# Performance work log

Measured on AMD Instinct MI355X. Metric: run time of the kernel, lower is better.

Reference implementation:

```python
import jax, jax.numpy as jnp
import numpy as np
import math

RCR = 5.2
RCA = 3.5
NUM_SPECIES = 4


def _triu_index(num_species):
    s1, s2 = np.triu_indices(num_species)
    ret = np.zeros((num_species, num_species), dtype=np.int32)
    ret[s1, s2] = np.arange(len(s1))
    ret[s2, s1] = np.arange(len(s1))
    return ret


def _cutoff_cosine(d, rc):
    return 0.5 * jnp.cos(d * (math.pi / rc)) + 0.5


def setup_inputs():
    key = jax.random.key(0)
    k1, k2 = jax.random.split(key)
    M, A = 32, 48
    BOX = 8.0  # ~0.43 atoms/A^3, realistic organic density
    coordinates = jax.random.uniform(k1, (M, A, 3), dtype=jnp.float32) * BOX
    species = jax.random.randint(k2, (M, A), 0, NUM_SPECIES)
    EtaR = jnp.array([16.0], dtype=jnp.float32)
    ShfR = jnp.asarray(0.9 + (RCR - 0.9) / 16.0 * np.arange(16), dtype=jnp.float32)
    EtaA = jnp.array([8.0], dtype=jnp.float32)
    Zeta = jnp.array([32.0], dtype=jnp.float32)
    ShfA = jnp.asarray(0.9 + (RCA - 0.9) / 4.0 * np.arange(4), dtype=jnp.float32)
    ShfZ = jnp.asarray((np.arange(8) + 0.5) * np.pi / 8.0, dtype=jnp.float32)
    return {"coordinates": coordinates, "EtaR": EtaR, "ShfR": ShfR,
            "EtaA": EtaA, "Zeta": Zeta, "ShfA": ShfA, "ShfZ": ShfZ,
            "species": species}


def _compute_aev(coordinates, EtaR, ShfR, EtaA, Zeta, ShfA, ShfZ, species):
    M, A, _ = coordinates.shape
    S = NUM_SPECIES
    npairs_sp = S * (S + 1) // 2  # 10 unordered species pairs
    rad_sub = EtaR.shape[0] * ShfR.shape[0]   # 16
    ang_sub = EtaA.shape[0] * Zeta.shape[0] * ShfA.shape[0] * ShfZ.shape[0]  # 32

    diff = coordinates[:, :, None, :] - coordinates[:, None, :, :]  # (M,A,A,3)
    D = jnp.linalg.norm(diff, axis=-1)                              # (M,A,A)
    mrow = jnp.arange(M)[:, None]

    # ---------- radial AEV (eq. 3) ----------
    p1, p2 = np.triu_indices(A, 1)                                  # static (P,)
    d = D[:, p1, p2]                                                # (M,P)
    mask_r = (d <= RCR).astype(d.dtype)
    du = d[:, :, None, None]                                        # (M,P,1,1)
    fc = _cutoff_cosine(du, RCR)
    rt = 0.25 * jnp.exp(-EtaR[:, None] * (du - ShfR[None, :]) ** 2) * fc
    rt = (rt * mask_r[:, :, None, None]).reshape(M, len(p1), rad_sub)
    sp = species
    idx1 = p1[None, :] * S + sp[:, p2]                              # (M,P)
    idx2 = p2[None, :] * S + sp[:, p1]
    radial = jnp.zeros((M, A * S, rad_sub), dtype=rt.dtype)
    radial = radial.at[mrow, idx1].add(rt).at[mrow, idx2].add(rt)
    radial = radial.reshape(M, A, S * rad_sub)

    # ---------- angular AEV (eq. 4) ----------
    # static triple list: central atom i with unordered neighbor pair (j,k), j,k != i
    jj, kk = np.triu_indices(A - 1, 1)
    tri = []
    for i in range(A):
        others = np.concatenate([np.arange(i), np.arange(i + 1, A)])
        tri.append(np.stack([np.full(jj.shape, i), others[jj], others[kk]], 1))
    tri = np.concatenate(tri)                                       # (T,3)
    ci, n1, n2 = tri[:, 0], tri[:, 1], tri[:, 2]

    v1 = coordinates[:, n1] - coordinates[:, ci]                    # (M,T,3)
    v2 = coordinates[:, n2] - coordinates[:, ci]
    d1 = D[:, ci, n1]
    d2 = D[:, ci, n2]
    mask_a = ((d1 <= RCA) & (d2 <= RCA)).astype(d1.dtype)           # (M,T)
    eps = 1e-8  # torch cosine_similarity eps
    cos = 0.95 * jnp.sum(v1 * v2, -1) / (jnp.maximum(d1, eps) * jnp.maximum(d2, eps))
    ang = jnp.arccos(cos)                                           # (M,T)

    # broadcast axes: (M, T, EtaA, Zeta, ShfA, ShfZ) as in torchani constants
    EtaA_b = EtaA.reshape(1, 1, -1, 1, 1, 1)
    Zeta_b = Zeta.reshape(1, 1, 1, -1, 1, 1)
    ShfA_b = ShfA.reshape(1, 1, 1, 1, -1, 1)
    ShfZ_b = ShfZ.reshape(1, 1, 1, 1, 1, -1)
    a6 = ang[:, :, None, None, None, None]
    dm = ((d1 + d2) / 2)[:, :, None, None, None, None]
    fcj = (_cutoff_cosine(d1, RCA) * _cutoff_cosine(d2, RCA))[:, :, None, None, None, None]
    f1 = ((1 + jnp.cos(a6 - ShfZ_b)) / 2) ** Zeta_b
    f2 = jnp.exp(-EtaA_b * (dm - ShfA_b) ** 2)
    at = (2 * f1 * f2 * fcj).reshape(M, tri.shape[0], ang_sub)
    at = at * mask_a[:, :, None]

    triu = jnp.asarray(_triu_index(S))
    pidx = triu[sp[:, n1], sp[:, n2]]                               # (M,T)
    flat = ci[None, :] * npairs_sp + pidx
    angular = jnp.zeros((M, A * npairs_sp, ang_sub), dtype=at.dtype)
    angular = angular.at[mrow, flat].add(at).reshape(M, A, npairs_sp * ang_sub)

    return jnp.concatenate([radial, angular], axis=-1)              # (M,A,384)


def reference(coordinates, EtaR, ShfR, EtaA, Zeta, ShfA, ShfZ, species):
    return _compute_aev(coordinates, EtaR, ShfR, EtaA, Zeta, ShfA, ShfZ, species)
```

## Files before the change

kernel.cpp:

```cpp
#include <hip/hip_runtime.h>
#include <hip/hip_bf16.h>


#define NA 48
#define RCR_F 5.2f
#define RCA_F 3.5f
#define PI_F 3.14159265358979f
#define LOG2E_F 1.44269504088896f
#define RADLEN 64
#define AEVLEN 384

#define WAVE_SYNC() do { asm volatile("s_waitcnt lgkmcnt(0)" ::: "memory"); \
                         __builtin_amdgcn_sched_barrier(0); } while (0)

struct Smem {
    float sx[NA], sy[NA], sz[NA];
    int   ssp[NA];
    float ra[NA]; unsigned rbu[NA];
    float ad[NA], avx[NA], avy[NA], avz[NA], afc[NA]; int asp[NA];
    float4 pstage[4][64];
    int    sortidx[4][64];
    float rpart[4][64];
    float apart[4][320];
};

template <typename T> __device__ __forceinline__ float toF(const T* p, int i);
template <> __device__ __forceinline__ float toF<float>(const float* p, int i) { return p[i]; }
template <> __device__ __forceinline__ float toF<__hip_bfloat16>(const __hip_bfloat16* p, int i) { return __bfloat162float(p[i]); }

template <typename T> __device__ __forceinline__ void stF(T* p, size_t i, float v);
template <> __device__ __forceinline__ void stF<float>(float* p, size_t i, float v) { p[i] = v; }
template <> __device__ __forceinline__ void stF<__hip_bfloat16>(__hip_bfloat16* p, size_t i, float v) { p[i] = __float2bfloat16(v); }

__device__ __forceinline__ int triu_idx(int a, int b) {
    int lo = a < b ? a : b;
    int hi = a < b ? b : a;
    return lo * 4 - (lo * (lo - 1)) / 2 + (hi - lo);
}

template <typename T>
__device__ void aev_body(Smem& sm,
    const T* __restrict__ coords, const T* __restrict__ etaR_p,
    const T* __restrict__ shfR_p, const T* __restrict__ etaA_p,
    const T* __restrict__ zeta_p, const T* __restrict__ shfA_p,
    const T* __restrict__ shfZ_p, const int* __restrict__ species,
    T* __restrict__ out)
{
    const int tid  = threadIdx.x;
    const int lane = tid & 63;
    const int w    = tid >> 6;
    const int bid  = blockIdx.x;
    const int m  = bid / NA;
    const int ci = bid % NA;

    const float etaR = toF(etaR_p, 0);
    const float etaA = toF(etaA_p, 0);
    const float zeta = toF(zeta_p, 0);
    const float kR   = etaR * LOG2E_F;
    const float k2   = etaA * LOG2E_F;

    if (tid < NA) {
        int g = m * NA + tid;
        sm.sx[tid]  = toF(coords, 3 * g + 0);
        sm.sy[tid]  = toF(coords, 3 * g + 1);
        sm.sz[tid]  = toF(coords, 3 * g + 2);
        sm.ssp[tid] = species[g];
    }
    __syncthreads();

    const float cx = sm.sx[ci], cy = sm.sy[ci], cz = sm.sz[ci];
    float dx = 0.f, dy = 0.f, dz = 0.f, d = 1e30f;
    if (lane < NA && lane != ci) {
        dx = sm.sx[lane] - cx; dy = sm.sy[lane] - cy; dz = sm.sz[lane] - cz;
        d = sqrtf(dx * dx + dy * dy + dz * dz);
    }
    const unsigned long long mRm = __ballot(d <= RCR_F);
    const unsigned long long mAm = __ballot(d <= RCA_F);
    const unsigned long long lanebit = 1ull << lane;
    const unsigned long long below = lanebit - 1ull;
    if (w == 0 && (mRm & lanebit)) {
        int s = __popcll(mRm & below);
        float fcR = 0.5f * __cosf(d * (PI_F / RCR_F)) + 0.5f;
        float rb = fmaxf(__log2f(0.25f * fcR) - kR * d * d, -8.0e4f);
        sm.ra[s]  = 2.f * kR * d;
        sm.rbu[s] = (__float_as_uint(rb) & ~3u) | (unsigned)sm.ssp[lane];
    }
    if (w == 1 && (mAm & lanebit)) {
        int s = __popcll(mAm & below);
        sm.ad[s]  = d;
        sm.avx[s] = dx; sm.avy[s] = dy; sm.avz[s] = dz;
        sm.afc[s] = 0.5f * __cosf(d * (PI_F / RCA_F)) + 0.5f;
        sm.asp[s] = sm.ssp[lane];
    }
    const int nR  = (int)__popcll(mRm);
    const int nAn = (int)__popcll(mAm);
    __syncthreads();

    const float myShfR = toF(shfR_p, lane & 15);
    const int   mySp   = lane >> 4;
    const float myRc   = kR * myShfR * myShfR;
    float racc = 0.f;
    for (int i = w; i < nR; i += 4) {
        unsigned ru = sm.rbu[i];
        float arg = __builtin_fmaf(sm.ra[i], myShfR, __uint_as_float(ru)) - myRc;
        float t = __builtin_amdgcn_exp2f(arg);
        racc += ((int)(ru & 3u) == mySp) ? t : 0.f;
    }
    sm.rpart[w][lane] = racc;

    const int myA = (lane >> 3) & 3;
    const int myZ = lane & 7;
    const int p0  = lane >> 5;
    const float myShfA = toF(shfA_p, myA);
    const float myShfZ = toF(shfZ_p, myZ);
    const float myCz = __cosf(myShfZ);
    const float mySz = __sinf(myShfZ);
    const float myLc = k2 * myShfA * myShfA;
    const bool  z32  = (zeta == 32.f);

    float accs[5] = {0.f, 0.f, 0.f, 0.f, 0.f};
    const int np = nAn * (nAn - 1) / 2;

    for (int base = 64 * w; base < np; base += 256) {
        const int nc = (np - base < 64) ? (np - base) : 64;
        const bool active = lane < nc;
        int myrow = -1;
        if (active) {
            int p = base + lane;
            const int b = 2 * nAn - 1;
            float sq = sqrtf((float)(b * b - 8 * p));
            int j = (int)(((float)b - sq) * 0.5f);
            if ((j + 1) * (b - 1 - j) <= 2 * p) j++;
            if (j * (b - j) > 2 * p) j--;
            int k = p - ((j * (b - j)) >> 1) + j + 1;

            float d1 = sm.ad[j], d2 = sm.ad[k];
            float dot = sm.avx[j] * sm.avx[k] + sm.avy[j] * sm.avy[k] + sm.avz[j] * sm.avz[k];
            float cv = 0.95f * dot / (fmaxf(d1, 1e-8f) * fmaxf(d2, 1e-8f));
            float sv = sqrtf(fmaxf(1.f - cv * cv, 0.f));
            float dm = 0.5f * (d1 + d2);
            float fc2 = 2.f * sm.afc[j] * sm.afc[k];
            float pe = fmaxf(-k2 * dm * dm + __log2f(fc2), -8.0e4f);
            float pd = 2.f * k2 * dm;
            sm.pstage[w][lane] = make_float4(cv, sv, pd, pe);
            myrow = triu_idx(sm.asp[j], sm.asp[k]);
        }

        int cnt[10], st[10];
        {
            int run = 0, rank = 0, stmy = 0;
            #pragma unroll
            for (int r = 0; r < 10; ++r) {
                unsigned long long bm = __ballot(myrow == r);
                bool mine = (myrow == r);
                rank = mine ? (int)__popcll(bm & below) : rank;
                stmy = mine ? run : stmy;
                st[r]  = run;
                cnt[r] = (int)__popcll(bm);
                run += cnt[r];
            }
            if (active) sm.sortidx[w][stmy + rank] = lane;
        }
        WAVE_SYNC();

        #pragma unroll
        for (int u = 0; u < 5; ++u) {
            const int cnE = cnt[2 * u], cnO = cnt[2 * u + 1];
            const int stE = st[2 * u],  stO = st[2 * u + 1];
            const int cnMy = p0 ? cnO : cnE;
            const int stMy = p0 ? stO : stE;
            const int trips = cnE > cnO ? cnE : cnO;
            for (int o = 0; o < trips; ++o) {
                bool valid = o < cnMy;
                int idx = valid ? (stMy + o) : 0;
                int q = sm.sortidx[w][idx];
                float4 P = sm.pstage[w][q];
                float cd = __builtin_fmaf(P.x, myCz, P.y * mySz);
                float x = __builtin_fmaf(0.5f, cd, 0.5f);
                float f1;
                if (z32) { float x2 = x*x, x4 = x2*x2, x8 = x4*x4, x16 = x8*x8; f1 = x16*x16; }
                else     { f1 = __powf(x, zeta); }
                float term = f1 * __builtin_amdgcn_exp2f(
                                 __builtin_fmaf(P.z, myShfA, P.w - myLc));
                accs[u] += valid ? term : 0.f;
            }
        }
        WAVE_SYNC();
    }

    sm.apart[w][lane + 0]   = accs[0];
    sm.apart[w][lane + 64]  = accs[1];
    sm.apart[w][lane + 128] = accs[2];
    sm.apart[w][lane + 192] = accs[3];
    sm.apart[w][lane + 256] = accs[4];
    __syncthreads();

    const size_t ob = (size_t)bid * AEVLEN;
    if (tid < 64) {
        float r = sm.rpart[0][tid] + sm.rpart[1][tid] + sm.rpart[2][tid] + sm.rpart[3][tid];
        stF(out, ob + tid, r);
    }
    {
        float v = sm.apart[0][tid] + sm.apart[1][tid] + sm.apart[2][tid] + sm.apart[3][tid];
        stF(out, ob + RADLEN + tid, v);
    }
    if (tid < 64) {
        int s = 256 + tid;
        float v = sm.apart[0][s] + sm.apart[1][s] + sm.apart[2][s] + sm.apart[3][s];
        stF(out, ob + RADLEN + s, v);
    }
}

__global__ __launch_bounds__(256) void aev_kernel(
    const void* coords, const void* etaR, const void* shfR, const void* etaA,
    const void* zeta, const void* shfA, const void* shfZ,
    const int* __restrict__ species, void* out)
{
    __shared__ Smem sm;
    const float probe = __uint_as_float(((const unsigned int*)shfR)[0]);
    if (probe > 0.85f && probe < 0.95f) {
        aev_body<float>(sm, (const float*)coords, (const float*)etaR,
                        (const float*)shfR, (const float*)etaA, (const float*)zeta,
                        (const float*)shfA, (const float*)shfZ, species, (float*)out);
    } else {
        aev_body<__hip_bfloat16>(sm, (const __hip_bfloat16*)coords,
                        (const __hip_bfloat16*)etaR, (const __hip_bfloat16*)shfR,
                        (const __hip_bfloat16*)etaA, (const __hip_bfloat16*)zeta,
                        (const __hip_bfloat16*)shfA, (const __hip_bfloat16*)shfZ,
                        species, (__hip_bfloat16*)out);
    }
}

extern "C" void kernel_launch(void* const* d_in, const int* in_sizes, int n_in,
                              void* d_out, int out_size, void* d_ws, size_t ws_size,
                              hipStream_t stream) {
    aev_kernel<<<dim3(32 * NA), dim3(256), 0, stream>>>(
        d_in[0], d_in[1], d_in[2], d_in[3], d_in[4], d_in[5], d_in[6],
        (const int*)d_in[7], d_out);
}
```

Measured before the change: 79.79 us.

## Pack LDS neighbor data into vector structs and write sorted pair params directly

Replaces the separate per-field LDS arrays with packed float2/float4 records, and takes the center-atom coordinates by wave shuffle from registers instead of staging through LDS, which removes one block barrier. Pair parameters are now written straight into their species-sorted slot, dropping the sortidx indirection and one dependent LDS read per inner iteration. Pairs are also interleaved across waves (p = base + 4*lane + w) to balance the tail. This cuts LDS traffic and latency in the angular loop, at the cost of wider LDS accesses and a changed order of the pair work.

```diff
diff --git a/kernel.cpp b/kernel.cpp
--- a/kernel.cpp
+++ b/kernel.cpp
@@ -14,14 +14,12 @@
                          __builtin_amdgcn_sched_barrier(0); } while (0)
 
 struct Smem {
-    float sx[NA], sy[NA], sz[NA];
-    int   ssp[NA];
-    float ra[NA]; unsigned rbu[NA];
-    float ad[NA], avx[NA], avy[NA], avz[NA], afc[NA]; int asp[NA];
+    float2 rr[NA];
+    float4 aj[NA];
+    float2 af[NA];
     float4 pstage[4][64];
-    int    sortidx[4][64];
-    float rpart[4][64];
-    float apart[4][320];
+    float  rpart[4][64];
+    float  apart[4][320];
 };
 
 template <typename T> __device__ __forceinline__ float toF(const T* p, int i);
@@ -59,19 +57,21 @@
     const float kR   = etaR * LOG2E_F;
     const float k2   = etaA * LOG2E_F;
 
-    if (tid < NA) {
-        int g = m * NA + tid;
-        sm.sx[tid]  = toF(coords, 3 * g + 0);
-        sm.sy[tid]  = toF(coords, 3 * g + 1);
-        sm.sz[tid]  = toF(coords, 3 * g + 2);
-        sm.ssp[tid] = species[g];
-    }
-    __syncthreads();
-
-    const float cx = sm.sx[ci], cy = sm.sy[ci], cz = sm.sz[ci];
+    float ax = 0.f, ay = 0.f, az = 0.f; int aspec = 0;
+    if (lane < NA) {
+        int g = m * NA + lane;
+        ax = toF(coords, 3 * g + 0);
+        ay = toF(coords, 3 * g + 1);
+        az = toF(coords, 3 * g + 2);
+        aspec = species[g];
+    }
+    const float cx = __shfl(ax, ci);
+    const float cy = __shfl(ay, ci);
+    const float cz = __shfl(az, ci);
+
     float dx = 0.f, dy = 0.f, dz = 0.f, d = 1e30f;
     if (lane < NA && lane != ci) {
-        dx = sm.sx[lane] - cx; dy = sm.sy[lane] - cy; dz = sm.sz[lane] - cz;
+        dx = ax - cx; dy = ay - cy; dz = az - cz;
         d = sqrtf(dx * dx + dy * dy + dz * dz);
     }
     const unsigned long long mRm = __ballot(d <= RCR_F);
@@ -82,15 +82,14 @@
         int s = __popcll(mRm & below);
         float fcR = 0.5f * __cosf(d * (PI_F / RCR_F)) + 0.5f;
         float rb = fmaxf(__log2f(0.25f * fcR) - kR * d * d, -8.0e4f);
-        sm.ra[s]  = 2.f * kR * d;
-        sm.rbu[s] = (__float_as_uint(rb) & ~3u) | (unsigned)sm.ssp[lane];
+        unsigned ru = (__float_as_uint(rb) & ~3u) | (unsigned)aspec;
+        sm.rr[s] = make_float2(2.f * kR * d, __uint_as_float(ru));
     }
     if (w == 1 && (mAm & lanebit)) {
         int s = __popcll(mAm & below);
-        sm.ad[s]  = d;
-        sm.avx[s] = dx; sm.avy[s] = dy; sm.avz[s] = dz;
-        sm.afc[s] = 0.5f * __cosf(d * (PI_F / RCA_F)) + 0.5f;
-        sm.asp[s] = sm.ssp[lane];
+        sm.aj[s] = make_float4(dx, dy, dz, d);
+        float fcA = 0.5f * __cosf(d * (PI_F / RCA_F)) + 0.5f;
+        sm.af[s] = make_float2(fcA, __uint_as_float((unsigned)aspec));
     }
     const int nR  = (int)__popcll(mRm);
     const int nAn = (int)__popcll(mAm);
@@ -101,10 +100,10 @@
     const float myRc   = kR * myShfR * myShfR;
     float racc = 0.f;
     for (int i = w; i < nR; i += 4) {
-        unsigned ru = sm.rbu[i];
-        float arg = __builtin_fmaf(sm.ra[i], myShfR, __uint_as_float(ru)) - myRc;
+        float2 rv = sm.rr[i];
+        float arg = __builtin_fmaf(rv.x, myShfR, rv.y) - myRc;
         float t = __builtin_amdgcn_exp2f(arg);
-        racc += ((int)(ru & 3u) == mySp) ? t : 0.f;
+        racc += ((int)(__float_as_uint(rv.y) & 3u) == mySp) ? t : 0.f;
     }
     sm.rpart[w][lane] = racc;
 
@@ -121,12 +120,12 @@
     float accs[5] = {0.f, 0.f, 0.f, 0.f, 0.f};
     const int np = nAn * (nAn - 1) / 2;
 
-    for (int base = 64 * w; base < np; base += 256) {
-        const int nc = (np - base < 64) ? (np - base) : 64;
-        const bool active = lane < nc;
+    for (int base = 0; base < np; base += 256) {
+        const int p = base + 4 * lane + w;
+        const bool active = p < np;
         int myrow = -1;
+        float cv = 0.f, sv = 0.f, pd = 0.f, pe = 0.f;
         if (active) {
-            int p = base + lane;
             const int b = 2 * nAn - 1;
             float sq = sqrtf((float)(b * b - 8 * p));
             int j = (int)(((float)b - sq) * 0.5f);
@@ -134,16 +133,17 @@
             if (j * (b - j) > 2 * p) j--;
             int k = p - ((j * (b - j)) >> 1) + j + 1;
 
-            float d1 = sm.ad[j], d2 = sm.ad[k];
-            float dot = sm.avx[j] * sm.avx[k] + sm.avy[j] * sm.avy[k] + sm.avz[j] * sm.avz[k];
-            float cv = 0.95f * dot / (fmaxf(d1, 1e-8f) * fmaxf(d2, 1e-8f));
-            float sv = sqrtf(fmaxf(1.f - cv * cv, 0.f));
+            float4 J = sm.aj[j], K = sm.aj[k];
+            float2 Jf = sm.af[j], Kf = sm.af[k];
+            float d1 = J.w, d2 = K.w;
+            float dot = J.x * K.x + J.y * K.y + J.z * K.z;
+            cv = 0.95f * dot / (fmaxf(d1, 1e-8f) * fmaxf(d2, 1e-8f));
+            sv = sqrtf(fmaxf(1.f - cv * cv, 0.f));
             float dm = 0.5f * (d1 + d2);
-            float fc2 = 2.f * sm.afc[j] * sm.afc[k];
-            float pe = fmaxf(-k2 * dm * dm + __log2f(fc2), -8.0e4f);
-            float pd = 2.f * k2 * dm;
-            sm.pstage[w][lane] = make_float4(cv, sv, pd, pe);
-            myrow = triu_idx(sm.asp[j], sm.asp[k]);
+            float fc2 = 2.f * Jf.x * Kf.x;
+            pe = fmaxf(-k2 * dm * dm + __log2f(fc2), -8.0e4f);
+            pd = 2.f * k2 * dm;
+            myrow = triu_idx((int)__float_as_uint(Jf.y), (int)__float_as_uint(Kf.y));
         }
 
         int cnt[10], st[10];
@@ -159,7 +159,7 @@
                 cnt[r] = (int)__popcll(bm);
                 run += cnt[r];
             }
-            if (active) sm.sortidx[w][stmy + rank] = lane;
+            if (active) sm.pstage[w][stmy + rank] = make_float4(cv, sv, pd, pe);
         }
         WAVE_SYNC();
 
@@ -173,8 +173,7 @@
             for (int o = 0; o < trips; ++o) {
                 bool valid = o < cnMy;
                 int idx = valid ? (stMy + o) : 0;
-                int q = sm.sortidx[w][idx];
-                float4 P = sm.pstage[w][q];
+                float4 P = sm.pstage[w][idx];
                 float cd = __builtin_fmaf(P.x, myCz, P.y * mySz);
                 float x = __builtin_fmaf(0.5f, cd, 0.5f);
                 float f1;
```

New measurement: 75.16 us. 1.06x faster.
